# Kernel optimization log

Measured on AMD Instinct MI355X. Metric: run time of the kernel, lower is better.

The kernel has to match this reference:

```python
import jax, jax.numpy as jnp
import numpy as np

POWER = 2.0
EPS = jnp.float32(np.finfo(np.float32).eps)


def setup_inputs() -> dict:
    key = jax.random.key(0)
    k1, k2, k3 = jax.random.split(key, 3)
    B, P, S = 2, 131072, 512
    station_coords = jax.random.uniform(k1, (B, S, 2), dtype=jnp.float32)
    station_values = jax.random.normal(k2, (B, S), dtype=jnp.float32)
    grid_points = jax.random.uniform(k3, (B, P, 2), dtype=jnp.float32)
    return {
        "station_coords": station_coords,
        "station_values": station_values,
        "grid_points": grid_points,
    }


def reference(station_coords, station_values, grid_points):
    # grid_points: (B, P, 2); station_coords: (B, S, 2)
    diff = grid_points[:, :, None, :] - station_coords[:, None, :, :]  # (B, P, S, 2)
    distances = jnp.sqrt(jnp.sum(diff * diff, axis=-1))                # (B, P, S)
    distances = jnp.where(distances == 0, EPS, distances)
    weights = 1.0 / distances ** POWER                                  # (B, P, S)
    weights_sum = jnp.sum(weights, axis=-1)                             # (B, P)
    interpolated = jnp.sum(weights * station_values[:, None, :], axis=-1) / weights_sum
    return interpolated  # (B, P)
```

## Files before the change

### kernel.cpp

```cpp
#include <hip/hip_runtime.h>


#define BLOCK 256
#define S_MAX 512
#define GPT 4

__global__ __launch_bounds__(BLOCK) void idw_kernel(
    const float* __restrict__ station_coords,
    const float* __restrict__ station_values,
    const float* __restrict__ grid_points,
    float* __restrict__ out,
    int P, int S) {

    __shared__ float st[S_MAX * 3];

    const int b = blockIdx.y;
    const float2* __restrict__ sc2 = (const float2*)(station_coords) + (size_t)b * S;
    const float*  __restrict__ svb = station_values + (size_t)b * S;

    for (int i = threadIdx.x; i < S; i += BLOCK) {
        const float2 c = sc2[i];
        st[3 * i + 0] = c.x;
        st[3 * i + 1] = c.y;
        st[3 * i + 2] = svb[i];
    }
    __syncthreads();

    const int tid = blockIdx.x * BLOCK + threadIdx.x;
    const float4* __restrict__ gp4 = (const float4*)grid_points + (size_t)b * (P / 2);
    const float4 ga = gp4[2 * tid + 0];
    const float4 gb = gp4[2 * tid + 1];
    const float gx0 = ga.x, gy0 = ga.y, gx1 = ga.z, gy1 = ga.w;
    const float gx2 = gb.x, gy2 = gb.y, gx3 = gb.z, gy3 = gb.w;

    constexpr float EPS  = 1.1920928955078125e-07f;
    constexpr float EPS2 = EPS * EPS;

    float ws0 = 0.0f, vs0 = 0.0f, ws1 = 0.0f, vs1 = 0.0f;
    float ws2 = 0.0f, vs2 = 0.0f, ws3 = 0.0f, vs3 = 0.0f;

    const float4* __restrict__ st4 = (const float4*)st;

    auto quad = [&](float gx, float gy, float& ws, float& vs,
                    const float4& f0, const float4& f1, const float4& f2) {
        const float dxa = gx - f0.x, dya = gy - f0.y;
        const float a = fmaf(dxa, dxa, fmaf(dya, dya, EPS2));
        const float dxb = gx - f0.w, dyb = gy - f1.x;
        const float bq = fmaf(dxb, dxb, fmaf(dyb, dyb, EPS2));
        const float dxc = gx - f1.z, dyc = gy - f1.w;
        const float c = fmaf(dxc, dxc, fmaf(dyc, dyc, EPS2));
        const float dxd = gx - f2.y, dyd = gy - f2.z;
        const float d = fmaf(dxd, dxd, fmaf(dyd, dyd, EPS2));
        const float pab = a * bq, pcd = c * d;
        const float sab = a + bq, scd = c + d;
        const float nab = fmaf(f1.y, a, f0.z * bq);
        const float ncd = fmaf(f2.w, c, f2.x * d);
        const float r = __builtin_amdgcn_rcpf(pab * pcd);
        ws = fmaf(fmaf(sab, pcd, scd * pab), r, ws);
        vs = fmaf(fmaf(nab, pcd, ncd * pab), r, vs);
    };

#pragma unroll 4
    for (int k = 0; k < S_MAX / 4; ++k) {
        const float4 f0 = st4[3 * k + 0];
        const float4 f1 = st4[3 * k + 1];
        const float4 f2 = st4[3 * k + 2];
        quad(gx0, gy0, ws0, vs0, f0, f1, f2);
        quad(gx1, gy1, ws1, vs1, f0, f1, f2);
        quad(gx2, gy2, ws2, vs2, f0, f1, f2);
        quad(gx3, gy3, ws3, vs3, f0, f1, f2);
    }

    const float4 res = make_float4(vs0 / ws0, vs1 / ws1, vs2 / ws2, vs3 / ws3);
    ((float4*)out)[(size_t)b * (P / 4) + tid] = res;
}

extern "C" void kernel_launch(void* const* d_in, const int* in_sizes, int n_in,
                              void* d_out, int out_size, void* d_ws, size_t ws_size,
                              hipStream_t stream) {
    const float* station_coords = (const float*)d_in[0];
    const float* station_values = (const float*)d_in[1];
    const float* grid_points    = (const float*)d_in[2];
    float* out = (float*)d_out;

    const int B = 2;
    const int S = in_sizes[1] / B;
    const int P = out_size / B;

    dim3 grid(P / (BLOCK * GPT), B);
    dim3 block(BLOCK);
    idw_kernel<<<grid, block, 0, stream>>>(station_coords, station_values,
                                           grid_points, out, P, S);
}
```

Before: 80.95 us.

## Combine sixteen stations per reciprocal and double-buffer LDS station loads

Extends the rational-combination trick from four to sixteen stations per reciprocal, merging partial numerators and denominators pairwise so that only one rcp is issued per sixteen stations per grid point. The station loop is manually double-buffered, loading the next 48 floats from LDS into registers while the current block is computed. Launch bounds now request one block per SM, which allows more registers. The risks are float overflow or underflow when multiplying sixteen squared distances, since values of order 2^-46 or up to about 2 can underflow the product, and higher register pressure.

```diff
diff --git a/kernel.cpp b/kernel.cpp
--- a/kernel.cpp
+++ b/kernel.cpp
@@ -5,7 +5,7 @@
 #define S_MAX 512
 #define GPT 4
 
-__global__ __launch_bounds__(BLOCK) void idw_kernel(
+__global__ __launch_bounds__(BLOCK, 1) void idw_kernel(
     const float* __restrict__ station_coords,
     const float* __restrict__ station_values,
     const float* __restrict__ grid_points,
@@ -41,8 +41,9 @@
 
     const float4* __restrict__ st4 = (const float4*)st;
 
-    auto quad = [&](float gx, float gy, float& ws, float& vs,
-                    const float4& f0, const float4& f1, const float4& f2) {
+    auto half4 = [&](float gx, float gy,
+                     const float4& f0, const float4& f1, const float4& f2,
+                     float& Pq, float& Wq, float& Vq) {
         const float dxa = gx - f0.x, dya = gy - f0.y;
         const float a = fmaf(dxa, dxa, fmaf(dya, dya, EPS2));
         const float dxb = gx - f0.w, dyb = gy - f1.x;
@@ -55,21 +56,55 @@
         const float sab = a + bq, scd = c + d;
         const float nab = fmaf(f1.y, a, f0.z * bq);
         const float ncd = fmaf(f2.w, c, f2.x * d);
-        const float r = __builtin_amdgcn_rcpf(pab * pcd);
-        ws = fmaf(fmaf(sab, pcd, scd * pab), r, ws);
-        vs = fmaf(fmaf(nab, pcd, ncd * pab), r, vs);
+        Wq = fmaf(sab, pcd, scd * pab);
+        Vq = fmaf(nab, pcd, ncd * pab);
+        Pq = pab * pcd;
     };
 
-#pragma unroll 4
-    for (int k = 0; k < S_MAX / 4; ++k) {
-        const float4 f0 = st4[3 * k + 0];
-        const float4 f1 = st4[3 * k + 1];
-        const float4 f2 = st4[3 * k + 2];
-        quad(gx0, gy0, ws0, vs0, f0, f1, f2);
-        quad(gx1, gy1, ws1, vs1, f0, f1, f2);
-        quad(gx2, gy2, ws2, vs2, f0, f1, f2);
-        quad(gx3, gy3, ws3, vs3, f0, f1, f2);
+    auto pair16 = [&](float gx, float gy, float& ws, float& vs,
+                      const float4 (&f)[12]) {
+        float P1, W1, V1, P2, W2, V2, P3, W3, V3, P4, W4, V4;
+        half4(gx, gy, f[0], f[1], f[2], P1, W1, V1);
+        half4(gx, gy, f[3], f[4], f[5], P2, W2, V2);
+        half4(gx, gy, f[6], f[7], f[8], P3, W3, V3);
+        half4(gx, gy, f[9], f[10], f[11], P4, W4, V4);
+        const float P12 = P1 * P2;
+        const float W12 = fmaf(W1, P2, W2 * P1);
+        const float V12 = fmaf(V1, P2, V2 * P1);
+        const float P34 = P3 * P4;
+        const float W34 = fmaf(W3, P4, W4 * P3);
+        const float V34 = fmaf(V3, P4, V4 * P3);
+        const float P16 = P12 * P34;
+        const float W16 = fmaf(W12, P34, W34 * P12);
+        const float V16 = fmaf(V12, P34, V34 * P12);
+        const float r = __builtin_amdgcn_rcpf(P16);
+        ws = fmaf(W16, r, ws);
+        vs = fmaf(V16, r, vs);
+    };
+
+    auto do4pts = [&](const float4 (&f)[12]) {
+        pair16(gx0, gy0, ws0, vs0, f);
+        pair16(gx1, gy1, ws1, vs1, f);
+        pair16(gx2, gy2, ws2, vs2, f);
+        pair16(gx3, gy3, ws3, vs3, f);
+    };
+
+    float4 cb[12], nb[12];
+#pragma unroll
+    for (int i = 0; i < 12; ++i) cb[i] = st4[i];
+
+    for (int j = 0; j < 15; ++j) {
+#pragma unroll
+        for (int i = 0; i < 12; ++i) nb[i] = st4[12 * (2 * j + 1) + i];
+        do4pts(cb);
+#pragma unroll
+        for (int i = 0; i < 12; ++i) cb[i] = st4[12 * (2 * j + 2) + i];
+        do4pts(nb);
     }
+#pragma unroll
+    for (int i = 0; i < 12; ++i) nb[i] = st4[12 * 31 + i];
+    do4pts(cb);
+    do4pts(nb);
 
     const float4 res = make_float4(vs0 / ws0, vs1 / ws1, vs2 / ws2, vs3 / ws3);
     ((float4*)out)[(size_t)b * (P / 4) + tid] = res;
```

Result: faster. 78.05 us (median of 2 runs) (-3.6%).
